# Optimization experiments

Hardware: AMD Instinct MI355X
Metric: run time of the kernel (lower is better)

## Reference

```python
import jax, jax.numpy as jnp
import numpy as np

# Fixed by module source / config defaults
L, H, D, DFF, T, B = 4, 4, 128, 512, 64, 1024
S, V, BOS = 4, 5, 4            # 4 orbital states, vocab 5, BOS token id 4
DH = D // H


def _ln(x, w, b):
    mu = x.mean(-1, keepdims=True)
    var = ((x - mu) ** 2).mean(-1, keepdims=True)
    return (x - mu) / jnp.sqrt(var + 1e-5) * w + b


def _decode(gumbel, state_emb, pos_emb, ln1_w, ln1_b, wqkv, bqkv, wo, bo,
            ln2_w, ln2_b, w1, b1, w2, b2, fn_w, fn_b, head_w, head_b,
            n_alpha, n_beta):
    def step(carry, xs):
        tok, a_rem, b_rem, Kc, Vc = carry
        g, i = xs                                   # g: (B,4), i: step index
        x = state_emb[tok] + pos_emb[i]             # (B, D)
        for l in range(L):
            # pre-LN causal self-attention with KV cache (torch MHA math)
            xn = _ln(x, ln1_w[l], ln1_b[l])
            q, k, v = jnp.split(xn @ wqkv[l].T + bqkv[l], 3, axis=-1)
            Kc = Kc.at[l, :, i].set(k)
            Vc = Vc.at[l, :, i].set(v)
            qh = q.reshape(B, H, DH)
            kh = Kc[l].reshape(B, T, H, DH)
            vh = Vc[l].reshape(B, T, H, DH)
            sc = jnp.einsum('bhd,bthd->bht', qh, kh) / jnp.sqrt(jnp.float32(DH))
            sc = jnp.where((jnp.arange(T) <= i)[None, None, :], sc, -jnp.inf)
            ctx = jnp.einsum('bht,bthd->bhd', jax.nn.softmax(sc, -1), vh).reshape(B, D)
            x = x + ctx @ wo[l].T + bo[l]
            # pre-LN FFN (exact GELU, matching nn.GELU default)
            h = jax.nn.gelu(_ln(x, ln2_w[l], ln2_b[l]) @ w1[l].T + b1[l], approximate=False)
            x = x + h @ w2[l].T + b2[l]
        logits = _ln(x, fn_w, fn_b) @ head_w.T + head_b   # (B, 4)
        # electron-budget validity mask (compute_validity_mask)
        oa = T - i - 1
        m = jnp.stack([
            (a_rem <= oa) & (b_rem <= oa),
            (b_rem > 0) & (a_rem <= oa) & (b_rem - 1 <= oa),
            (a_rem > 0) & (a_rem - 1 <= oa) & (b_rem <= oa),
            (a_rem > 0) & (b_rem > 0) & (a_rem - 1 <= oa) & (b_rem - 1 <= oa)], -1)
        logp = jax.nn.log_softmax(jnp.where(m, logits, -jnp.inf), -1)
        s = jnp.argmax(logp + g, -1)                # gumbel-max == multinomial
        lp = jnp.take_along_axis(logp, s[:, None], 1)[:, 0]
        return (s, a_rem - (s >> 1), b_rem - (s & 1), Kc, Vc), (s, lp)

    tok0 = jnp.full((B,), BOS, jnp.int32)
    a0 = jnp.full((B,), n_alpha, jnp.int32)
    b0 = jnp.full((B,), n_beta, jnp.int32)
    Kc0 = jnp.zeros((L, B, T, D), jnp.float32)
    Vc0 = jnp.zeros((L, B, T, D), jnp.float32)
    _, (states, lps) = jax.lax.scan(
        step, (tok0, a0, b0, Kc0, Vc0), (gumbel.transpose(1, 0, 2), jnp.arange(T)))
    return states.T, lps.sum(0)                      # (B, T) states, (B,) log-prob


def setup_inputs() -> dict:
    key = jax.random.key(0)
    ks = jax.random.split(key, 10)
    p = lambda k, shp: jax.random.normal(k, shp, jnp.float32) * 0.02
    u = jax.random.uniform(ks[0], (B, T, S), jnp.float32, 1e-6, 1.0 - 1e-6)
    return {
        'gumbel': -jnp.log(-jnp.log(u)),
        'state_emb': p(ks[1], (V, D)),
        'pos_emb': p(ks[2], (T + 1, D)),
        'ln1_w': jnp.ones((L, D)), 'ln1_b': jnp.zeros((L, D)),
        'wqkv': p(ks[3], (L, 3 * D, D)), 'bqkv': jnp.zeros((L, 3 * D)),
        'wo': p(ks[4], (L, D, D)), 'bo': jnp.zeros((L, D)),
        'ln2_w': jnp.ones((L, D)), 'ln2_b': jnp.zeros((L, D)),
        'w1': p(ks[5], (L, DFF, D)), 'b1': jnp.zeros((L, DFF)),
        'w2': p(ks[6], (L, D, DFF)), 'b2': jnp.zeros((L, D)),
        'fn_w': jnp.ones((D,)), 'fn_b': jnp.zeros((D,)),
        'head_w': p(ks[7], (S, D)), 'head_b': jnp.zeros((S,)),
        'n_alpha': 16, 'n_beta': 16,
    }


def reference(gumbel, state_emb, pos_emb, ln1_w, ln1_b, wqkv, bqkv, wo, bo,
              ln2_w, ln2_b, w1, b1, w2, b2, fn_w, fn_b, head_w, head_b,
              n_alpha, n_beta):
    return _decode(gumbel, state_emb, pos_emb, ln1_w, ln1_b, wqkv, bqkv, wo, bo,
                   ln2_w, ln2_b, w1, b1, w2, b2, fn_w, fn_b, head_w, head_b,
                   n_alpha, n_beta)
```

## Files before the change

### kernel.cpp

```cpp
#include <hip/hip_runtime.h>
#include <math.h>

namespace {
constexpr int L_ = 4, H_ = 4, D_ = 128, DFF_ = 512, T_ = 64, B_ = 1024;
constexpr int S_ = 4, BOS_ = 4, DH_ = 32;
constexpr int NB = 4;
constexpr int NBLK = B_ / NB;
constexpr int NTH = 1024;

constexpr size_t KC_BLK = (size_t)L_ * NB * T_ * D_;
constexpr size_t KC_OFF = 0;
constexpr size_t VC_OFF = KC_OFF + (size_t)NBLK * KC_BLK;
}

__device__ __forceinline__ float4 ld4(const float* p) {
  return *reinterpret_cast<const float4*>(p);
}

__device__ __forceinline__ float gelu_exact(float v) {
  return 0.5f * v * (1.0f + erff(v * 0.70710678118654752440f));
}

#define SEL4(a, e) ((e) == 0 ? (a)[0] : (e) == 1 ? (a)[1] : (e) == 2 ? (a)[2] : (a)[3])

__device__ __forceinline__ void ln_wave(const float* __restrict__ src,
                                        float* __restrict__ dst,
                                        const float* __restrict__ w,
                                        const float* __restrict__ b, int lane) {
  float v0 = src[lane], v1 = src[lane + 64];
  float s = v0 + v1;
#pragma unroll
  for (int off = 32; off > 0; off >>= 1) s += __shfl_xor(s, off);
  float mu = s * (1.f / 128.f);
  float d0 = v0 - mu, d1 = v1 - mu;
  float s2 = d0 * d0 + d1 * d1;
#pragma unroll
  for (int off = 32; off > 0; off >>= 1) s2 += __shfl_xor(s2, off);
  float inv = 1.f / sqrtf(s2 * (1.f / 128.f) + 1e-5f);
  dst[lane] = d0 * inv * w[lane] + b[lane];
  dst[lane + 64] = d1 * inv * w[lane + 64] + b[lane + 64];
}

__global__ __launch_bounds__(NTH) void decode_kernel(
    const float* __restrict__ gumbel, const float* __restrict__ state_emb,
    const float* __restrict__ pos_emb,
    const float* __restrict__ ln1w, const float* __restrict__ ln1b,
    const float* __restrict__ wqkv, const float* __restrict__ bqkv,
    const float* __restrict__ wo, const float* __restrict__ bo,
    const float* __restrict__ ln2w, const float* __restrict__ ln2b,
    const float* __restrict__ w1, const float* __restrict__ b1,
    const float* __restrict__ w2, const float* __restrict__ b2,
    const float* __restrict__ fnw, const float* __restrict__ fnb,
    const float* __restrict__ headw, const float* __restrict__ headb,
    const int* __restrict__ nalpha, const int* __restrict__ nbeta,
    float* __restrict__ ws, float* __restrict__ out) {
  const int tid = threadIdx.x;
  const int blk = blockIdx.x;
  const int lane = tid & 63;
  const int w = tid >> 6;
  const int og = tid >> 3;
  const int k8 = tid & 7;

  float* Kc = ws + KC_OFF + (size_t)blk * KC_BLK;
  float* Vc = ws + VC_OFF + (size_t)blk * KC_BLK;

  __shared__ __align__(16) float xres[NB][D_];
  __shared__ __align__(16) float xn[NB][D_];
  __shared__ __align__(16) float qb[NB][D_];
  __shared__ __align__(16) float hbuf[NB][DFF_];
  __shared__ float sc[NB][H_][T_];
  __shared__ float logits[NB][S_];
  __shared__ int tok[NB];

  int arem_r = 0, brem_r = 0;
  float lps_r = 0.f;
  if (tid < NB) {
    tok[tid] = BOS_;
    arem_r = nalpha[0];
    brem_r = nbeta[0];
  }
  __syncthreads();

  for (int i = 0; i < T_; ++i) {
    if (tid < 512) {
      const int e = tid >> 7, d = tid & 127;
      xres[e][d] = state_emb[tok[e] * D_ + d] + pos_emb[i * D_ + d];
    }
    __syncthreads();

    for (int l = 0; l < L_; ++l) {
      if (w < NB) ln_wave(xres[w], xn[w], ln1w + l * D_, ln1b + l * D_, lane);
      __syncthreads();

      {
        float aq[4] = {0.f, 0.f, 0.f, 0.f};
        float ak[4] = {0.f, 0.f, 0.f, 0.f};
        float av[4] = {0.f, 0.f, 0.f, 0.f};
        const float* wq = wqkv + ((size_t)l * 384 + og) * D_;
        const float* wk = wq + (size_t)128 * D_;
        const float* wv = wq + (size_t)256 * D_;
#pragma unroll
        for (int m = 0; m < 4; ++m) {
          const int f4 = k8 + 8 * m;
          const float4 q4 = ld4(wq + 4 * f4);
          const float4 k4v = ld4(wk + 4 * f4);
          const float4 v4 = ld4(wv + 4 * f4);
#pragma unroll
          for (int e = 0; e < 4; ++e) {
            const float4 x4 = ld4(&xn[e][4 * f4]);
            aq[e] += q4.x * x4.x + q4.y * x4.y + q4.z * x4.z + q4.w * x4.w;
            ak[e] += k4v.x * x4.x + k4v.y * x4.y + k4v.z * x4.z + k4v.w * x4.w;
            av[e] += v4.x * x4.x + v4.y * x4.y + v4.z * x4.z + v4.w * x4.w;
          }
        }
#pragma unroll
        for (int e = 0; e < 4; ++e) {
          aq[e] += __shfl_xor(aq[e], 1); aq[e] += __shfl_xor(aq[e], 2); aq[e] += __shfl_xor(aq[e], 4);
          ak[e] += __shfl_xor(ak[e], 1); ak[e] += __shfl_xor(ak[e], 2); ak[e] += __shfl_xor(ak[e], 4);
          av[e] += __shfl_xor(av[e], 1); av[e] += __shfl_xor(av[e], 2); av[e] += __shfl_xor(av[e], 4);
        }
        const size_t kvb = ((size_t)l * NB) * T_ * D_ + (size_t)i * D_ + og;
        if (k8 < 4) {
          const int e = k8;
          qb[e][og] = SEL4(aq, e) + bqkv[l * 384 + og];
          Vc[kvb + (size_t)e * T_ * D_] = SEL4(av, e) + bqkv[l * 384 + 256 + og];
        } else {
          const int e = k8 - 4;
          Kc[kvb + (size_t)e * T_ * D_] = SEL4(ak, e) + bqkv[l * 384 + 128 + og];
        }
      }
      __syncthreads();

      {
        const int e = w >> 2, h = w & 3;
        const int t = lane;
        float s0 = -INFINITY;
        {
          const float4* q4 = reinterpret_cast<const float4*>(&qb[e][h * DH_]);
          const float* kp = Kc + (((size_t)l * NB + e) * T_ + t) * D_ + h * DH_;
          float a = 0.f;
#pragma unroll
          for (int k = 0; k < 8; ++k) {
            const float4 qv = q4[k];
            const float4 kv = ld4(kp + 4 * k);
            a += qv.x * kv.x + qv.y * kv.y + qv.z * kv.z + qv.w * kv.w;
          }
          if (t <= i) s0 = a * 0.17677669529663687f;
        }
        float mx = s0;
#pragma unroll
        for (int off = 32; off > 0; off >>= 1) mx = fmaxf(mx, __shfl_xor(mx, off));
        float p = expf(s0 - mx);
        float sum = p;
#pragma unroll
        for (int off = 32; off > 0; off >>= 1) sum += __shfl_xor(sum, off);
        sc[e][h][t] = p / sum;

        const int j = lane & 31, thalf = lane >> 5;
        const float* vp = Vc + (((size_t)l * NB + e) * T_ + thalf * 32) * D_ + h * DH_ + j;
        const float* pp = &sc[e][h][thalf * 32];
        float acc = 0.f;
#pragma unroll
        for (int m2 = 0; m2 < 32; ++m2) {
          acc += pp[m2] * vp[(size_t)m2 * D_];
        }
        acc += __shfl_xor(acc, 32);
        if (thalf == 0) qb[e][h * DH_ + j] = acc;
      }
      __syncthreads();

      {
        float ac[4] = {0.f, 0.f, 0.f, 0.f};
        const float* wrow = wo + ((size_t)l * D_ + og) * D_;
#pragma unroll
        for (int m = 0; m < 4; ++m) {
          const int f4 = k8 + 8 * m;
          const float4 w4 = ld4(wrow + 4 * f4);
#pragma unroll
          for (int e = 0; e < 4; ++e) {
            const float4 x4 = ld4(&qb[e][4 * f4]);
            ac[e] += w4.x * x4.x + w4.y * x4.y + w4.z * x4.z + w4.w * x4.w;
          }
        }
#pragma unroll
        for (int e = 0; e < 4; ++e) {
          ac[e] += __shfl_xor(ac[e], 1); ac[e] += __shfl_xor(ac[e], 2); ac[e] += __shfl_xor(ac[e], 4);
        }
        if (k8 < 4) {
          const int e = k8;
          xres[e][og] += SEL4(ac, e) + bo[l * D_ + og];
        }
      }
      __syncthreads();

      if (w < NB) ln_wave(xres[w], xn[w], ln2w + l * D_, ln2b + l * D_, lane);
      __syncthreads();

      {
        float ac[4][4];
#pragma unroll
        for (int r = 0; r < 4; ++r)
#pragma unroll
          for (int e = 0; e < 4; ++e) ac[r][e] = 0.f;
        const float* wb = w1 + ((size_t)l * DFF_ + og) * D_;
#pragma unroll
        for (int m = 0; m < 4; ++m) {
          const int f4 = k8 + 8 * m;
          float4 wr[4];
#pragma unroll
          for (int r = 0; r < 4; ++r) wr[r] = ld4(wb + (size_t)(128 * r) * D_ + 4 * f4);
#pragma unroll
          for (int e = 0; e < 4; ++e) {
            const float4 x4 = ld4(&xn[e][4 * f4]);
#pragma unroll
            for (int r = 0; r < 4; ++r) {
              ac[r][e] += wr[r].x * x4.x + wr[r].y * x4.y + wr[r].z * x4.z + wr[r].w * x4.w;
            }
          }
        }
#pragma unroll
        for (int r = 0; r < 4; ++r)
#pragma unroll
          for (int e = 0; e < 4; ++e) {
            ac[r][e] += __shfl_xor(ac[r][e], 1);
            ac[r][e] += __shfl_xor(ac[r][e], 2);
            ac[r][e] += __shfl_xor(ac[r][e], 4);
          }
        if (k8 < 4) {
          const int e = k8;
          hbuf[e][og] = gelu_exact(SEL4(ac[0], e) + b1[l * DFF_ + og]);
          hbuf[e][og + 128] = gelu_exact(SEL4(ac[1], e) + b1[l * DFF_ + og + 128]);
        } else {
          const int e = k8 - 4;
          hbuf[e][og + 256] = gelu_exact(SEL4(ac[2], e) + b1[l * DFF_ + og + 256]);
          hbuf[e][og + 384] = gelu_exact(SEL4(ac[3], e) + b1[l * DFF_ + og + 384]);
        }
      }
      __syncthreads();

      {
        float ac[4] = {0.f, 0.f, 0.f, 0.f};
        const float* wrow = w2 + ((size_t)l * D_ + og) * DFF_;
#pragma unroll
        for (int m = 0; m < 16; ++m) {
          const int f4 = k8 + 8 * m;
          const float4 w4 = ld4(wrow + 4 * f4);
#pragma unroll
          for (int e = 0; e < 4; ++e) {
            const float4 h4 = ld4(&hbuf[e][4 * f4]);
            ac[e] += w4.x * h4.x + w4.y * h4.y + w4.z * h4.z + w4.w * h4.w;
          }
        }
#pragma unroll
        for (int e = 0; e < 4; ++e) {
          ac[e] += __shfl_xor(ac[e], 1); ac[e] += __shfl_xor(ac[e], 2); ac[e] += __shfl_xor(ac[e], 4);
        }
        if (k8 < 4) {
          const int e = k8;
          xres[e][og] += SEL4(ac, e) + b2[l * D_ + og];
        }
      }
      __syncthreads();
    }

    if (w < NB) ln_wave(xres[w], xn[w], fnw, fnb, lane);
    __syncthreads();

    if (tid < 512) {
      const int e = tid >> 7, rest = tid & 127, s = rest >> 5, j = rest & 31;
      const float4 a = ld4(&xn[e][4 * j]);
      const float4 hw = ld4(headw + s * D_ + 4 * j);
      float acc = a.x * hw.x + a.y * hw.y + a.z * hw.z + a.w * hw.w;
#pragma unroll
      for (int off = 1; off < 32; off <<= 1) acc += __shfl_xor(acc, off);
      if (j == 0) logits[e][s] = acc + headb[s];
    }
    __syncthreads();

    if (tid < NB) {
      const int e = tid;
      const int b = blk * NB + e;
      const int a = arem_r, bb = brem_r;
      const int oa = T_ - 1 - i;
      bool m[4];
      m[0] = (a <= oa) && (bb <= oa);
      m[1] = (bb > 0) && (a <= oa) && (bb - 1 <= oa);
      m[2] = (a > 0) && (a - 1 <= oa) && (bb <= oa);
      m[3] = (a > 0) && (bb > 0) && (a - 1 <= oa) && (bb - 1 <= oa);
      float mx = -INFINITY;
#pragma unroll
      for (int s = 0; s < 4; ++s)
        if (m[s]) mx = fmaxf(mx, logits[e][s]);
      float sum = 0.f;
      float lg[4];
#pragma unroll
      for (int s = 0; s < 4; ++s) {
        if (m[s]) {
          const float z = logits[e][s] - mx;
          sum += expf(z);
          lg[s] = z;
        } else {
          lg[s] = -INFINITY;
        }
      }
      const float lse = logf(sum);
      float best = -INFINITY;
      int bs = 0;
#pragma unroll
      for (int s = 0; s < 4; ++s) {
        const float lp = lg[s] - lse;
        const float y = lp + gumbel[((size_t)b * T_ + i) * S_ + s];
        if (y > best) { best = y; bs = s; }
      }
      lps_r += SEL4(lg, bs) - lse;
      out[(size_t)b * T_ + i] = (float)bs;
      tok[e] = bs;
      arem_r = a - (bs >> 1);
      brem_r = bb - (bs & 1);
    }
    __syncthreads();
  }

  if (tid < NB) out[(size_t)B_ * T_ + blk * NB + tid] = lps_r;
}

extern "C" void kernel_launch(void* const* d_in, const int* in_sizes, int n_in,
                              void* d_out, int out_size, void* d_ws, size_t ws_size,
                              hipStream_t stream) {
  const float* gumbel    = (const float*)d_in[0];
  const float* state_emb = (const float*)d_in[1];
  const float* pos_emb   = (const float*)d_in[2];
  const float* ln1w      = (const float*)d_in[3];
  const float* ln1b      = (const float*)d_in[4];
  const float* wqkv      = (const float*)d_in[5];
  const float* bqkv      = (const float*)d_in[6];
  const float* wo        = (const float*)d_in[7];
  const float* bo        = (const float*)d_in[8];
  const float* ln2w      = (const float*)d_in[9];
  const float* ln2b      = (const float*)d_in[10];
  const float* w1        = (const float*)d_in[11];
  const float* b1        = (const float*)d_in[12];
  const float* w2        = (const float*)d_in[13];
  const float* b2        = (const float*)d_in[14];
  const float* fnw       = (const float*)d_in[15];
  const float* fnb       = (const float*)d_in[16];
  const float* headw     = (const float*)d_in[17];
  const float* headb     = (const float*)d_in[18];
  const int* nalpha      = (const int*)d_in[19];
  const int* nbeta       = (const int*)d_in[20];
  float* ws = (float*)d_ws;
  float* out = (float*)d_out;

  decode_kernel<<<dim3(NBLK), dim3(NTH), 0, stream>>>(
      gumbel, state_emb, pos_emb, ln1w, ln1b, wqkv, bqkv, wo, bo, ln2w, ln2b,
      w1, b1, w2, b2, fnw, fnb, headw, headb, nalpha, nbeta, ws, out);
}
```

Baseline: 9.241 ms.

## Split block into per-sequence wave groups with atomic sub-barriers and head-major KV cache

Reassigns work so each group of four waves owns one sequence, with each wave handling one attention head and a slice of every projection. Block-wide __syncthreads are replaced by a spin barrier on a per-sequence shared-memory counter, so the four sequences in a block no longer wait on each other. The KV cache moves to a head-major layout so each wave's K/V rows are contiguous. Redundant layernorm and sampling now run in every wave, the attention loop skips masked timesteps, and the custom atomic barrier with sleep adds polling overhead and memory-ordering risk. Weight reuse also drops: each weight row is now loaded for one sequence instead of being shared across four.

```diff
diff --git a/kernel.cpp b/kernel.cpp
--- a/kernel.cpp
+++ b/kernel.cpp
@@ -8,9 +8,8 @@
 constexpr int NBLK = B_ / NB;
 constexpr int NTH = 1024;
 
-constexpr size_t KC_BLK = (size_t)L_ * NB * T_ * D_;
-constexpr size_t KC_OFF = 0;
-constexpr size_t VC_OFF = KC_OFF + (size_t)NBLK * KC_BLK;
+constexpr size_t KC_BLK = (size_t)L_ * NB * H_ * T_ * DH_;
+constexpr size_t VC_OFF = (size_t)NBLK * KC_BLK;
 }
 
 __device__ __forceinline__ float4 ld4(const float* p) {
@@ -23,10 +22,24 @@
 
 #define SEL4(a, e) ((e) == 0 ? (a)[0] : (e) == 1 ? (a)[1] : (e) == 2 ? (a)[2] : (a)[3])
 
-__device__ __forceinline__ void ln_wave(const float* __restrict__ src,
-                                        float* __restrict__ dst,
-                                        const float* __restrict__ w,
-                                        const float* __restrict__ b, int lane) {
+__device__ __forceinline__ void gbar(int* cnt, int lane) {
+  int tgt = 0;
+  if (lane == 0) {
+    int my = __hip_atomic_fetch_add(cnt, 1, __ATOMIC_RELEASE,
+                                    __HIP_MEMORY_SCOPE_WORKGROUP);
+    tgt = (my & ~3) + 4;
+  }
+  tgt = __shfl(tgt, 0);
+  while (__hip_atomic_load(cnt, __ATOMIC_ACQUIRE,
+                           __HIP_MEMORY_SCOPE_WORKGROUP) < tgt) {
+    __builtin_amdgcn_s_sleep(1);
+  }
+}
+
+__device__ __forceinline__ void ln_red(const float* __restrict__ src,
+                                       float* __restrict__ dst,
+                                       const float* __restrict__ w,
+                                       const float* __restrict__ b, int lane) {
   float v0 = src[lane], v1 = src[lane + 64];
   float s = v0 + v1;
 #pragma unroll
@@ -58,94 +71,105 @@
   const int blk = blockIdx.x;
   const int lane = tid & 63;
   const int w = tid >> 6;
-  const int og = tid >> 3;
-  const int k8 = tid & 7;
-
-  float* Kc = ws + KC_OFF + (size_t)blk * KC_BLK;
+  const int e = w >> 2;
+  const int h = w & 3;
+  const int og8 = lane >> 3;
+  const int k8 = lane & 7;
+
+  float* Kc = ws + (size_t)blk * KC_BLK;
   float* Vc = ws + VC_OFF + (size_t)blk * KC_BLK;
 
   __shared__ __align__(16) float xres[NB][D_];
   __shared__ __align__(16) float xn[NB][D_];
-  __shared__ __align__(16) float qb[NB][D_];
+  __shared__ __align__(16) float ctx[NB][D_];
   __shared__ __align__(16) float hbuf[NB][DFF_];
-  __shared__ float sc[NB][H_][T_];
+  __shared__ __align__(16) float qs[NB][H_][DH_];
+  __shared__ float ps[NB][H_][T_];
   __shared__ float logits[NB][S_];
-  __shared__ int tok[NB];
-
-  int arem_r = 0, brem_r = 0;
+  __shared__ int cnt[NB];
+
+  int bs_cur = BOS_;
+  int arem_r = nalpha[0], brem_r = nbeta[0];
   float lps_r = 0.f;
-  if (tid < NB) {
-    tok[tid] = BOS_;
-    arem_r = nalpha[0];
-    brem_r = nbeta[0];
-  }
+  if (tid < NB) cnt[tid] = 0;
   __syncthreads();
 
   for (int i = 0; i < T_; ++i) {
-    if (tid < 512) {
-      const int e = tid >> 7, d = tid & 127;
-      xres[e][d] = state_emb[tok[e] * D_ + d] + pos_emb[i * D_ + d];
+    if (lane < 32) {
+      const int d = h * 32 + lane;
+      xres[e][d] = state_emb[bs_cur * D_ + d] + pos_emb[i * D_ + d];
     }
-    __syncthreads();
+    gbar(&cnt[e], lane);
 
     for (int l = 0; l < L_; ++l) {
-      if (w < NB) ln_wave(xres[w], xn[w], ln1w + l * D_, ln1b + l * D_, lane);
-      __syncthreads();
+      ln_red(xres[e], xn[e], ln1w + l * D_, ln1b + l * D_, lane);
 
       {
-        float aq[4] = {0.f, 0.f, 0.f, 0.f};
-        float ak[4] = {0.f, 0.f, 0.f, 0.f};
-        float av[4] = {0.f, 0.f, 0.f, 0.f};
-        const float* wq = wqkv + ((size_t)l * 384 + og) * D_;
-        const float* wk = wq + (size_t)128 * D_;
-        const float* wv = wq + (size_t)256 * D_;
-#pragma unroll
-        for (int m = 0; m < 4; ++m) {
-          const int f4 = k8 + 8 * m;
-          const float4 q4 = ld4(wq + 4 * f4);
-          const float4 k4v = ld4(wk + 4 * f4);
-          const float4 v4 = ld4(wv + 4 * f4);
-#pragma unroll
-          for (int e = 0; e < 4; ++e) {
+        const float* wq = wqkv + ((size_t)l * 384 + h * 32) * D_;
+        const float* wk = wqkv + ((size_t)l * 384 + 128 + h * 32) * D_;
+        const float* wv = wqkv + ((size_t)l * 384 + 256 + h * 32) * D_;
+        const size_t cb = (((size_t)(l * NB + e) * H_ + h) * T_ + i) * DH_;
+#pragma unroll
+        for (int rg = 0; rg < 4; ++rg) {
+          const int r = rg * 8 + og8;
+          const float* wr = wq + (size_t)r * D_;
+          float acc = 0.f;
+#pragma unroll
+          for (int m = 0; m < 4; ++m) {
+            const int f4 = k8 + 8 * m;
+            const float4 w4 = ld4(wr + 4 * f4);
             const float4 x4 = ld4(&xn[e][4 * f4]);
-            aq[e] += q4.x * x4.x + q4.y * x4.y + q4.z * x4.z + q4.w * x4.w;
-            ak[e] += k4v.x * x4.x + k4v.y * x4.y + k4v.z * x4.z + k4v.w * x4.w;
-            av[e] += v4.x * x4.x + v4.y * x4.y + v4.z * x4.z + v4.w * x4.w;
+            acc += w4.x * x4.x + w4.y * x4.y + w4.z * x4.z + w4.w * x4.w;
           }
-        }
-#pragma unroll
-        for (int e = 0; e < 4; ++e) {
-          aq[e] += __shfl_xor(aq[e], 1); aq[e] += __shfl_xor(aq[e], 2); aq[e] += __shfl_xor(aq[e], 4);
-          ak[e] += __shfl_xor(ak[e], 1); ak[e] += __shfl_xor(ak[e], 2); ak[e] += __shfl_xor(ak[e], 4);
-          av[e] += __shfl_xor(av[e], 1); av[e] += __shfl_xor(av[e], 2); av[e] += __shfl_xor(av[e], 4);
-        }
-        const size_t kvb = ((size_t)l * NB) * T_ * D_ + (size_t)i * D_ + og;
-        if (k8 < 4) {
-          const int e = k8;
-          qb[e][og] = SEL4(aq, e) + bqkv[l * 384 + og];
-          Vc[kvb + (size_t)e * T_ * D_] = SEL4(av, e) + bqkv[l * 384 + 256 + og];
-        } else {
-          const int e = k8 - 4;
-          Kc[kvb + (size_t)e * T_ * D_] = SEL4(ak, e) + bqkv[l * 384 + 128 + og];
-        }
-      }
-      __syncthreads();
+          acc += __shfl_xor(acc, 1); acc += __shfl_xor(acc, 2); acc += __shfl_xor(acc, 4);
+          if (k8 == 0) qs[e][h][r] = acc + bqkv[l * 384 + h * 32 + r];
+        }
+#pragma unroll
+        for (int rg = 0; rg < 4; ++rg) {
+          const int r = rg * 8 + og8;
+          const float* wr = wk + (size_t)r * D_;
+          float acc = 0.f;
+#pragma unroll
+          for (int m = 0; m < 4; ++m) {
+            const int f4 = k8 + 8 * m;
+            const float4 w4 = ld4(wr + 4 * f4);
+            const float4 x4 = ld4(&xn[e][4 * f4]);
+            acc += w4.x * x4.x + w4.y * x4.y + w4.z * x4.z + w4.w * x4.w;
+          }
+          acc += __shfl_xor(acc, 1); acc += __shfl_xor(acc, 2); acc += __shfl_xor(acc, 4);
+          if (k8 == 0) Kc[cb + r] = acc + bqkv[l * 384 + 128 + h * 32 + r];
+        }
+#pragma unroll
+        for (int rg = 0; rg < 4; ++rg) {
+          const int r = rg * 8 + og8;
+          const float* wr = wv + (size_t)r * D_;
+          float acc = 0.f;
+#pragma unroll
+          for (int m = 0; m < 4; ++m) {
+            const int f4 = k8 + 8 * m;
+            const float4 w4 = ld4(wr + 4 * f4);
+            const float4 x4 = ld4(&xn[e][4 * f4]);
+            acc += w4.x * x4.x + w4.y * x4.y + w4.z * x4.z + w4.w * x4.w;
+          }
+          acc += __shfl_xor(acc, 1); acc += __shfl_xor(acc, 2); acc += __shfl_xor(acc, 4);
+          if (k8 == 0) Vc[cb + r] = acc + bqkv[l * 384 + 256 + h * 32 + r];
+        }
+      }
+      asm volatile("s_waitcnt vmcnt(0)" ::: "memory");
 
       {
-        const int e = w >> 2, h = w & 3;
         const int t = lane;
         float s0 = -INFINITY;
-        {
-          const float4* q4 = reinterpret_cast<const float4*>(&qb[e][h * DH_]);
-          const float* kp = Kc + (((size_t)l * NB + e) * T_ + t) * D_ + h * DH_;
+        if (t <= i) {
+          const float* kp = Kc + (((size_t)(l * NB + e) * H_ + h) * T_ + t) * DH_;
           float a = 0.f;
 #pragma unroll
           for (int k = 0; k < 8; ++k) {
-            const float4 qv = q4[k];
+            const float4 qv = ld4(&qs[e][h][4 * k]);
             const float4 kv = ld4(kp + 4 * k);
             a += qv.x * kv.x + qv.y * kv.y + qv.z * kv.z + qv.w * kv.w;
           }
-          if (t <= i) s0 = a * 0.17677669529663687f;
+          s0 = a * 0.17677669529663687f;
         }
         float mx = s0;
 #pragma unroll
@@ -154,148 +178,103 @@
         float sum = p;
 #pragma unroll
         for (int off = 32; off > 0; off >>= 1) sum += __shfl_xor(sum, off);
-        sc[e][h][t] = p / sum;
+        ps[e][h][t] = p / sum;
 
         const int j = lane & 31, thalf = lane >> 5;
-        const float* vp = Vc + (((size_t)l * NB + e) * T_ + thalf * 32) * D_ + h * DH_ + j;
-        const float* pp = &sc[e][h][thalf * 32];
+        const float* vp = Vc + (((size_t)(l * NB + e) * H_ + h) * T_) * DH_ + j;
+        const float* pp = &ps[e][h][thalf * 32];
         float acc = 0.f;
 #pragma unroll
-        for (int m2 = 0; m2 < 32; ++m2) {
-          acc += pp[m2] * vp[(size_t)m2 * D_];
+        for (int m = 0; m < 32; ++m) {
+          if (thalf * 32 + m <= i) acc += pp[m] * vp[(size_t)(thalf * 32 + m) * DH_];
         }
         acc += __shfl_xor(acc, 32);
-        if (thalf == 0) qb[e][h * DH_ + j] = acc;
-      }
-      __syncthreads();
-
-      {
-        float ac[4] = {0.f, 0.f, 0.f, 0.f};
-        const float* wrow = wo + ((size_t)l * D_ + og) * D_;
+        if (thalf == 0) ctx[e][h * 32 + j] = acc;
+      }
+      gbar(&cnt[e], lane);
+
+#pragma unroll
+      for (int rg = 0; rg < 4; ++rg) {
+        const int r = h * 32 + rg * 8 + og8;
+        const float* wr = wo + ((size_t)l * D_ + r) * D_;
+        float acc = 0.f;
 #pragma unroll
         for (int m = 0; m < 4; ++m) {
           const int f4 = k8 + 8 * m;
-          const float4 w4 = ld4(wrow + 4 * f4);
-#pragma unroll
-          for (int e = 0; e < 4; ++e) {
-            const float4 x4 = ld4(&qb[e][4 * f4]);
-            ac[e] += w4.x * x4.x + w4.y * x4.y + w4.z * x4.z + w4.w * x4.w;
-          }
-        }
-#pragma unroll
-        for (int e = 0; e < 4; ++e) {
-          ac[e] += __shfl_xor(ac[e], 1); ac[e] += __shfl_xor(ac[e], 2); ac[e] += __shfl_xor(ac[e], 4);
-        }
-        if (k8 < 4) {
-          const int e = k8;
-          xres[e][og] += SEL4(ac, e) + bo[l * D_ + og];
-        }
-      }
-      __syncthreads();
-
-      if (w < NB) ln_wave(xres[w], xn[w], ln2w + l * D_, ln2b + l * D_, lane);
-      __syncthreads();
-
-      {
-        float ac[4][4];
-#pragma unroll
-        for (int r = 0; r < 4; ++r)
-#pragma unroll
-          for (int e = 0; e < 4; ++e) ac[r][e] = 0.f;
-        const float* wb = w1 + ((size_t)l * DFF_ + og) * D_;
+          const float4 w4 = ld4(wr + 4 * f4);
+          const float4 x4 = ld4(&ctx[e][4 * f4]);
+          acc += w4.x * x4.x + w4.y * x4.y + w4.z * x4.z + w4.w * x4.w;
+        }
+        acc += __shfl_xor(acc, 1); acc += __shfl_xor(acc, 2); acc += __shfl_xor(acc, 4);
+        if (k8 == 0) xres[e][r] += acc + bo[l * D_ + r];
+      }
+      gbar(&cnt[e], lane);
+
+      ln_red(xres[e], xn[e], ln2w + l * D_, ln2b + l * D_, lane);
+
+#pragma unroll 4
+      for (int rg = 0; rg < 16; ++rg) {
+        const int r = h * 128 + rg * 8 + og8;
+        const float* wr = w1 + ((size_t)l * DFF_ + r) * D_;
+        float acc = 0.f;
 #pragma unroll
         for (int m = 0; m < 4; ++m) {
           const int f4 = k8 + 8 * m;
-          float4 wr[4];
-#pragma unroll
-          for (int r = 0; r < 4; ++r) wr[r] = ld4(wb + (size_t)(128 * r) * D_ + 4 * f4);
-#pragma unroll
-          for (int e = 0; e < 4; ++e) {
-            const float4 x4 = ld4(&xn[e][4 * f4]);
-#pragma unroll
-            for (int r = 0; r < 4; ++r) {
-              ac[r][e] += wr[r].x * x4.x + wr[r].y * x4.y + wr[r].z * x4.z + wr[r].w * x4.w;
-            }
-          }
-        }
-#pragma unroll
-        for (int r = 0; r < 4; ++r)
-#pragma unroll
-          for (int e = 0; e < 4; ++e) {
-            ac[r][e] += __shfl_xor(ac[r][e], 1);
-            ac[r][e] += __shfl_xor(ac[r][e], 2);
-            ac[r][e] += __shfl_xor(ac[r][e], 4);
-          }
-        if (k8 < 4) {
-          const int e = k8;
-          hbuf[e][og] = gelu_exact(SEL4(ac[0], e) + b1[l * DFF_ + og]);
-          hbuf[e][og + 128] = gelu_exact(SEL4(ac[1], e) + b1[l * DFF_ + og + 128]);
-        } else {
-          const int e = k8 - 4;
-          hbuf[e][og + 256] = gelu_exact(SEL4(ac[2], e) + b1[l * DFF_ + og + 256]);
-          hbuf[e][og + 384] = gelu_exact(SEL4(ac[3], e) + b1[l * DFF_ + og + 384]);
-        }
-      }
-      __syncthreads();
-
-      {
-        float ac[4] = {0.f, 0.f, 0.f, 0.f};
-        const float* wrow = w2 + ((size_t)l * D_ + og) * DFF_;
+          const float4 w4 = ld4(wr + 4 * f4);
+          const float4 x4 = ld4(&xn[e][4 * f4]);
+          acc += w4.x * x4.x + w4.y * x4.y + w4.z * x4.z + w4.w * x4.w;
+        }
+        acc += __shfl_xor(acc, 1); acc += __shfl_xor(acc, 2); acc += __shfl_xor(acc, 4);
+        if (k8 == 0) hbuf[e][r] = gelu_exact(acc + b1[l * DFF_ + r]);
+      }
+      gbar(&cnt[e], lane);
+
+#pragma unroll
+      for (int rg = 0; rg < 4; ++rg) {
+        const int r = h * 32 + rg * 8 + og8;
+        const float* wr = w2 + ((size_t)l * D_ + r) * DFF_;
+        float acc = 0.f;
 #pragma unroll
         for (int m = 0; m < 16; ++m) {
           const int f4 = k8 + 8 * m;
-          const float4 w4 = ld4(wrow + 4 * f4);
-#pragma unroll
-          for (int e = 0; e < 4; ++e) {
-            const float4 h4 = ld4(&hbuf[e][4 * f4]);
-            ac[e] += w4.x * h4.x + w4.y * h4.y + w4.z * h4.z + w4.w * h4.w;
-          }
-        }
-#pragma unroll
-        for (int e = 0; e < 4; ++e) {
-          ac[e] += __shfl_xor(ac[e], 1); ac[e] += __shfl_xor(ac[e], 2); ac[e] += __shfl_xor(ac[e], 4);
-        }
-        if (k8 < 4) {
-          const int e = k8;
-          xres[e][og] += SEL4(ac, e) + b2[l * D_ + og];
-        }
-      }
-      __syncthreads();
+          const float4 w4 = ld4(wr + 4 * f4);
+          const float4 x4 = ld4(&hbuf[e][4 * f4]);
+          acc += w4.x * x4.x + w4.y * x4.y + w4.z * x4.z + w4.w * x4.w;
+        }
+        acc += __shfl_xor(acc, 1); acc += __shfl_xor(acc, 2); acc += __shfl_xor(acc, 4);
+        if (k8 == 0) xres[e][r] += acc + b2[l * D_ + r];
+      }
+      gbar(&cnt[e], lane);
     }
 
-    if (w < NB) ln_wave(xres[w], xn[w], fnw, fnb, lane);
-    __syncthreads();
-
-    if (tid < 512) {
-      const int e = tid >> 7, rest = tid & 127, s = rest >> 5, j = rest & 31;
-      const float4 a = ld4(&xn[e][4 * j]);
-      const float4 hw = ld4(headw + s * D_ + 4 * j);
-      float acc = a.x * hw.x + a.y * hw.y + a.z * hw.z + a.w * hw.w;
-#pragma unroll
-      for (int off = 1; off < 32; off <<= 1) acc += __shfl_xor(acc, off);
-      if (j == 0) logits[e][s] = acc + headb[s];
+    ln_red(xres[e], xn[e], fnw, fnb, lane);
+
+    {
+      float v = xn[e][lane] * headw[h * D_ + lane] +
+                xn[e][lane + 64] * headw[h * D_ + lane + 64];
+#pragma unroll
+      for (int off = 32; off > 0; off >>= 1) v += __shfl_xor(v, off);
+      if (lane == 0) logits[e][h] = v + headb[h];
     }
-    __syncthreads();
-
-    if (tid < NB) {
-      const int e = tid;
-      const int b = blk * NB + e;
+    gbar(&cnt[e], lane);
+
+    {
       const int a = arem_r, bb = brem_r;
       const int oa = T_ - 1 - i;
-      bool m[4];
-      m[0] = (a <= oa) && (bb <= oa);
-      m[1] = (bb > 0) && (a <= oa) && (bb - 1 <= oa);
-      m[2] = (a > 0) && (a - 1 <= oa) && (bb <= oa);
-      m[3] = (a > 0) && (bb > 0) && (a - 1 <= oa) && (bb - 1 <= oa);
+      bool mk[4];
+      mk[0] = (a <= oa) && (bb <= oa);
+      mk[1] = (bb > 0) && (a <= oa) && (bb - 1 <= oa);
+      mk[2] = (a > 0) && (a - 1 <= oa) && (bb <= oa);
+      mk[3] = (a > 0) && (bb > 0) && (a - 1 <= oa) && (bb - 1 <= oa);
       float mx = -INFINITY;
 #pragma unroll
       for (int s = 0; s < 4; ++s)
-        if (m[s]) mx = fmaxf(mx, logits[e][s]);
+        if (mk[s]) mx = fmaxf(mx, logits[e][s]);
       float sum = 0.f;
       float lg[4];
 #pragma unroll
       for (int s = 0; s < 4; ++s) {
-        if (m[s]) {
+        if (mk[s]) {
           const float z = logits[e][s] - mx;
           sum += expf(z);
           lg[s] = z;
@@ -304,24 +283,23 @@
         }
       }
       const float lse = logf(sum);
+      const size_t gb = ((size_t)(blk * NB + e) * T_ + i) * S_;
       float best = -INFINITY;
       int bs = 0;
 #pragma unroll
       for (int s = 0; s < 4; ++s) {
-        const float lp = lg[s] - lse;
-        const float y = lp + gumbel[((size_t)b * T_ + i) * S_ + s];
+        const float y = (lg[s] - lse) + gumbel[gb + s];
         if (y > best) { best = y; bs = s; }
       }
       lps_r += SEL4(lg, bs) - lse;
-      out[(size_t)b * T_ + i] = (float)bs;
-      tok[e] = bs;
+      if (w == e * 4 && lane == 0) out[(size_t)(blk * NB + e) * T_ + i] = (float)bs;
+      bs_cur = bs;
       arem_r = a - (bs >> 1);
       brem_r = bb - (bs & 1);
     }
-    __syncthreads();
   }
 
-  if (tid < NB) out[(size_t)B_ * T_ + blk * NB + tid] = lps_r;
+  if (h == 0 && lane == 0) out[(size_t)B_ * T_ + blk * NB + e] = lps_r;
 }
 
 extern "C" void kernel_launch(void* const* d_in, const int* in_sizes, int n_in,
```

Result: slower. 22.88 ms (+147.6%).

## Halve sequences per block to two and skip masked causal attention work

Applied to the files above, without the earlier changes.

Each block now handles two sequences with 512 threads instead of four with 1024, giving 512 blocks. Every matvec is rewritten so each 8-lane group computes two output rows for both sequences. Attention also skips the QK dot products and the PV accumulation for positions past the current step. The aim is more blocks in flight and less wasted causal work, but weight rows are now re-read from cache for only two sequences per block instead of four.

```diff
diff --git a/kernel.cpp b/kernel.cpp
--- a/kernel.cpp
+++ b/kernel.cpp
@@ -4,13 +4,12 @@
 namespace {
 constexpr int L_ = 4, H_ = 4, D_ = 128, DFF_ = 512, T_ = 64, B_ = 1024;
 constexpr int S_ = 4, BOS_ = 4, DH_ = 32;
-constexpr int NB = 4;
+constexpr int NB = 2;
 constexpr int NBLK = B_ / NB;
-constexpr int NTH = 1024;
+constexpr int NTH = 512;
 
 constexpr size_t KC_BLK = (size_t)L_ * NB * T_ * D_;
-constexpr size_t KC_OFF = 0;
-constexpr size_t VC_OFF = KC_OFF + (size_t)NBLK * KC_BLK;
+constexpr size_t VC_OFF = (size_t)NBLK * KC_BLK;
 }
 
 __device__ __forceinline__ float4 ld4(const float* p) {
@@ -20,8 +19,6 @@
 __device__ __forceinline__ float gelu_exact(float v) {
   return 0.5f * v * (1.0f + erff(v * 0.70710678118654752440f));
 }
-
-#define SEL4(a, e) ((e) == 0 ? (a)[0] : (e) == 1 ? (a)[1] : (e) == 2 ? (a)[2] : (a)[3])
 
 __device__ __forceinline__ void ln_wave(const float* __restrict__ src,
                                         float* __restrict__ dst,
@@ -40,6 +37,8 @@
   dst[lane] = d0 * inv * w[lane] + b[lane];
   dst[lane + 64] = d1 * inv * w[lane + 64] + b[lane + 64];
 }
+
+#define RED8(a) { a += __shfl_xor(a, 1); a += __shfl_xor(a, 2); a += __shfl_xor(a, 4); }
 
 __global__ __launch_bounds__(NTH) void decode_kernel(
     const float* __restrict__ gumbel, const float* __restrict__ state_emb,
@@ -61,14 +60,14 @@
   const int og = tid >> 3;
   const int k8 = tid & 7;
 
-  float* Kc = ws + KC_OFF + (size_t)blk * KC_BLK;
+  float* Kc = ws + (size_t)blk * KC_BLK;
   float* Vc = ws + VC_OFF + (size_t)blk * KC_BLK;
 
   __shared__ __align__(16) float xres[NB][D_];
   __shared__ __align__(16) float xn[NB][D_];
   __shared__ __align__(16) float qb[NB][D_];
   __shared__ __align__(16) float hbuf[NB][DFF_];
-  __shared__ float sc[NB][H_][T_];
+  __shared__ float ps[NB][H_][T_];
   __shared__ float logits[NB][S_];
   __shared__ int tok[NB];
 
@@ -82,7 +81,7 @@
   __syncthreads();
 
   for (int i = 0; i < T_; ++i) {
-    if (tid < 512) {
+    if (tid < NB * D_) {
       const int e = tid >> 7, d = tid & 127;
       xres[e][d] = state_emb[tok[e] * D_ + d] + pos_emb[i * D_ + d];
     }
@@ -93,40 +92,54 @@
       __syncthreads();
 
       {
-        float aq[4] = {0.f, 0.f, 0.f, 0.f};
-        float ak[4] = {0.f, 0.f, 0.f, 0.f};
-        float av[4] = {0.f, 0.f, 0.f, 0.f};
-        const float* wq = wqkv + ((size_t)l * 384 + og) * D_;
-        const float* wk = wq + (size_t)128 * D_;
-        const float* wv = wq + (size_t)256 * D_;
+        float aq0[2] = {0.f, 0.f}, aq1[2] = {0.f, 0.f};
+        float ak0[2] = {0.f, 0.f}, ak1[2] = {0.f, 0.f};
+        float av0[2] = {0.f, 0.f}, av1[2] = {0.f, 0.f};
+        const float* wb = wqkv + (size_t)l * 384 * D_;
 #pragma unroll
         for (int m = 0; m < 4; ++m) {
           const int f4 = k8 + 8 * m;
-          const float4 q4 = ld4(wq + 4 * f4);
-          const float4 k4v = ld4(wk + 4 * f4);
-          const float4 v4 = ld4(wv + 4 * f4);
-#pragma unroll
-          for (int e = 0; e < 4; ++e) {
-            const float4 x4 = ld4(&xn[e][4 * f4]);
-            aq[e] += q4.x * x4.x + q4.y * x4.y + q4.z * x4.z + q4.w * x4.w;
-            ak[e] += k4v.x * x4.x + k4v.y * x4.y + k4v.z * x4.z + k4v.w * x4.w;
-            av[e] += v4.x * x4.x + v4.y * x4.y + v4.z * x4.z + v4.w * x4.w;
-          }
-        }
-#pragma unroll
-        for (int e = 0; e < 4; ++e) {
-          aq[e] += __shfl_xor(aq[e], 1); aq[e] += __shfl_xor(aq[e], 2); aq[e] += __shfl_xor(aq[e], 4);
-          ak[e] += __shfl_xor(ak[e], 1); ak[e] += __shfl_xor(ak[e], 2); ak[e] += __shfl_xor(ak[e], 4);
-          av[e] += __shfl_xor(av[e], 1); av[e] += __shfl_xor(av[e], 2); av[e] += __shfl_xor(av[e], 4);
-        }
-        const size_t kvb = ((size_t)l * NB) * T_ * D_ + (size_t)i * D_ + og;
-        if (k8 < 4) {
-          const int e = k8;
-          qb[e][og] = SEL4(aq, e) + bqkv[l * 384 + og];
-          Vc[kvb + (size_t)e * T_ * D_] = SEL4(av, e) + bqkv[l * 384 + 256 + og];
-        } else {
-          const int e = k8 - 4;
-          Kc[kvb + (size_t)e * T_ * D_] = SEL4(ak, e) + bqkv[l * 384 + 128 + og];
+          const float4 x0 = ld4(&xn[0][4 * f4]);
+          const float4 x1 = ld4(&xn[1][4 * f4]);
+          const float4 wq0 = ld4(wb + (size_t)(og) * D_ + 4 * f4);
+          const float4 wq1 = ld4(wb + (size_t)(og + 64) * D_ + 4 * f4);
+          const float4 wk0 = ld4(wb + (size_t)(og + 128) * D_ + 4 * f4);
+          const float4 wk1 = ld4(wb + (size_t)(og + 192) * D_ + 4 * f4);
+          const float4 wv0 = ld4(wb + (size_t)(og + 256) * D_ + 4 * f4);
+          const float4 wv1 = ld4(wb + (size_t)(og + 320) * D_ + 4 * f4);
+          aq0[0] += wq0.x * x0.x + wq0.y * x0.y + wq0.z * x0.z + wq0.w * x0.w;
+          aq0[1] += wq0.x * x1.x + wq0.y * x1.y + wq0.z * x1.z + wq0.w * x1.w;
+          aq1[0] += wq1.x * x0.x + wq1.y * x0.y + wq1.z * x0.z + wq1.w * x0.w;
+          aq1[1] += wq1.x * x1.x + wq1.y * x1.y + wq1.z * x1.z + wq1.w * x1.w;
+          ak0[0] += wk0.x * x0.x + wk0.y * x0.y + wk0.z * x0.z + wk0.w * x0.w;
+          ak0[1] += wk0.x * x1.x + wk0.y * x1.y + wk0.z * x1.z + wk0.w * x1.w;
+          ak1[0] += wk1.x * x0.x + wk1.y * x0.y + wk1.z * x0.z + wk1.w * x0.w;
+          ak1[1] += wk1.x * x1.x + wk1.y * x1.y + wk1.z * x1.z + wk1.w * x1.w;
+          av0[0] += wv0.x * x0.x + wv0.y * x0.y + wv0.z * x0.z + wv0.w * x0.w;
+          av0[1] += wv0.x * x1.x + wv0.y * x1.y + wv0.z * x1.z + wv0.w * x1.w;
+          av1[0] += wv1.x * x0.x + wv1.y * x0.y + wv1.z * x0.z + wv1.w * x0.w;
+          av1[1] += wv1.x * x1.x + wv1.y * x1.y + wv1.z * x1.z + wv1.w * x1.w;
+        }
+        RED8(aq0[0]); RED8(aq0[1]); RED8(aq1[0]); RED8(aq1[1]);
+        RED8(ak0[0]); RED8(ak0[1]); RED8(ak1[0]); RED8(ak1[1]);
+        RED8(av0[0]); RED8(av0[1]); RED8(av1[0]); RED8(av1[1]);
+        const float* bq = bqkv + l * 384;
+        if (k8 == 0) {
+          const size_t cb = (((size_t)l * NB + 0) * T_ + i) * D_;
+          qb[0][og] = aq0[0] + bq[og];
+          qb[0][og + 64] = aq1[0] + bq[og + 64];
+          Kc[cb + og] = ak0[0] + bq[og + 128];
+          Kc[cb + og + 64] = ak1[0] + bq[og + 192];
+          Vc[cb + og] = av0[0] + bq[og + 256];
+          Vc[cb + og + 64] = av1[0] + bq[og + 320];
+        } else if (k8 == 1) {
+          const size_t cb = (((size_t)l * NB + 1) * T_ + i) * D_;
+          qb[1][og] = aq0[1] + bq[og];
+          qb[1][og + 64] = aq1[1] + bq[og + 64];
+          Kc[cb + og] = ak0[1] + bq[og + 128];
+          Kc[cb + og + 64] = ak1[1] + bq[og + 192];
+          Vc[cb + og] = av0[1] + bq[og + 256];
+          Vc[cb + og + 64] = av1[1] + bq[og + 320];
         }
       }
       __syncthreads();
@@ -135,7 +148,7 @@
         const int e = w >> 2, h = w & 3;
         const int t = lane;
         float s0 = -INFINITY;
-        {
+        if (t <= i) {
           const float4* q4 = reinterpret_cast<const float4*>(&qb[e][h * DH_]);
           const float* kp = Kc + (((size_t)l * NB + e) * T_ + t) * D_ + h * DH_;
           float a = 0.f;
@@ -145,7 +158,7 @@
             const float4 kv = ld4(kp + 4 * k);
             a += qv.x * kv.x + qv.y * kv.y + qv.z * kv.z + qv.w * kv.w;
           }
-          if (t <= i) s0 = a * 0.17677669529663687f;
+          s0 = a * 0.17677669529663687f;
         }
         float mx = s0;
 #pragma unroll
@@ -154,15 +167,15 @@
         float sum = p;
 #pragma unroll
         for (int off = 32; off > 0; off >>= 1) sum += __shfl_xor(sum, off);
-        sc[e][h][t] = p / sum;
+        ps[e][h][t] = p / sum;
 
         const int j = lane & 31, thalf = lane >> 5;
         const float* vp = Vc + (((size_t)l * NB + e) * T_ + thalf * 32) * D_ + h * DH_ + j;
-        const float* pp = &sc[e][h][thalf * 32];
+        const float* pp = &ps[e][h][thalf * 32];
         float acc = 0.f;
 #pragma unroll
-        for (int m2 = 0; m2 < 32; ++m2) {
-          acc += pp[m2] * vp[(size_t)m2 * D_];
+        for (int m = 0; m < 32; ++m) {
+          if (thalf * 32 + m <= i) acc += pp[m] * vp[(size_t)m * D_];
         }
         acc += __shfl_xor(acc, 32);
         if (thalf == 0) qb[e][h * DH_ + j] = acc;
@@ -170,25 +183,27 @@
       __syncthreads();
 
       {
-        float ac[4] = {0.f, 0.f, 0.f, 0.f};
-        const float* wrow = wo + ((size_t)l * D_ + og) * D_;
+        float a0[2] = {0.f, 0.f}, a1[2] = {0.f, 0.f};
+        const float* wb = wo + (size_t)l * D_ * D_;
 #pragma unroll
         for (int m = 0; m < 4; ++m) {
           const int f4 = k8 + 8 * m;
-          const float4 w4 = ld4(wrow + 4 * f4);
-#pragma unroll
-          for (int e = 0; e < 4; ++e) {
-            const float4 x4 = ld4(&qb[e][4 * f4]);
-            ac[e] += w4.x * x4.x + w4.y * x4.y + w4.z * x4.z + w4.w * x4.w;
-          }
-        }
-#pragma unroll
-        for (int e = 0; e < 4; ++e) {
-          ac[e] += __shfl_xor(ac[e], 1); ac[e] += __shfl_xor(ac[e], 2); ac[e] += __shfl_xor(ac[e], 4);
-        }
-        if (k8 < 4) {
-          const int e = k8;
-          xres[e][og] += SEL4(ac, e) + bo[l * D_ + og];
+          const float4 x0 = ld4(&qb[0][4 * f4]);
+          const float4 x1 = ld4(&qb[1][4 * f4]);
+          const float4 w0 = ld4(wb + (size_t)(og) * D_ + 4 * f4);
+          const float4 w1v = ld4(wb + (size_t)(og + 64) * D_ + 4 * f4);
+          a0[0] += w0.x * x0.x + w0.y * x0.y + w0.z * x0.z + w0.w * x0.w;
+          a0[1] += w0.x * x1.x + w0.y * x1.y + w0.z * x1.z + w0.w * x1.w;
+          a1[0] += w1v.x * x0.x + w1v.y * x0.y + w1v.z * x0.z + w1v.w * x0.w;
+          a1[1] += w1v.x * x1.x + w1v.y * x1.y + w1v.z * x1.z + w1v.w * x1.w;
+        }
+        RED8(a0[0]); RED8(a0[1]); RED8(a1[0]); RED8(a1[1]);
+        if (k8 == 0) {
+          xres[0][og] += a0[0] + bo[l * D_ + og];
+          xres[0][og + 64] += a1[0] + bo[l * D_ + og + 64];
+        } else if (k8 == 1) {
+          xres[1][og] += a0[1] + bo[l * D_ + og];
+          xres[1][og + 64] += a1[1] + bo[l * D_ + og + 64];
         }
       }
       __syncthreads();
@@ -197,67 +212,62 @@
       __syncthreads();
 
       {
-        float ac[4][4];
-#pragma unroll
-        for (int r = 0; r < 4; ++r)
-#pragma unroll
-          for (int e = 0; e < 4; ++e) ac[r][e] = 0.f;
-        const float* wb = w1 + ((size_t)l * DFF_ + og) * D_;
+        float ac[8][2];
+#pragma unroll
+        for (int r = 0; r < 8; ++r) { ac[r][0] = 0.f; ac[r][1] = 0.f; }
+        const float* wb = w1 + (size_t)l * DFF_ * D_;
 #pragma unroll
         for (int m = 0; m < 4; ++m) {
           const int f4 = k8 + 8 * m;
-          float4 wr[4];
-#pragma unroll
-          for (int r = 0; r < 4; ++r) wr[r] = ld4(wb + (size_t)(128 * r) * D_ + 4 * f4);
-#pragma unroll
-          for (int e = 0; e < 4; ++e) {
-            const float4 x4 = ld4(&xn[e][4 * f4]);
-#pragma unroll
-            for (int r = 0; r < 4; ++r) {
-              ac[r][e] += wr[r].x * x4.x + wr[r].y * x4.y + wr[r].z * x4.z + wr[r].w * x4.w;
-            }
+          const float4 x0 = ld4(&xn[0][4 * f4]);
+          const float4 x1 = ld4(&xn[1][4 * f4]);
+#pragma unroll
+          for (int r = 0; r < 8; ++r) {
+            const float4 w4 = ld4(wb + (size_t)(og + 64 * r) * D_ + 4 * f4);
+            ac[r][0] += w4.x * x0.x + w4.y * x0.y + w4.z * x0.z + w4.w * x0.w;
+            ac[r][1] += w4.x * x1.x + w4.y * x1.y + w4.z * x1.z + w4.w * x1.w;
           }
         }
 #pragma unroll
-        for (int r = 0; r < 4; ++r)
-#pragma unroll
-          for (int e = 0; e < 4; ++e) {
-            ac[r][e] += __shfl_xor(ac[r][e], 1);
-            ac[r][e] += __shfl_xor(ac[r][e], 2);
-            ac[r][e] += __shfl_xor(ac[r][e], 4);
+        for (int r = 0; r < 8; ++r) { RED8(ac[r][0]); RED8(ac[r][1]); }
+        if (k8 == 0) {
+#pragma unroll
+          for (int r = 0; r < 8; ++r) {
+            const int o = og + 64 * r;
+            hbuf[0][o] = gelu_exact(ac[r][0] + b1[l * DFF_ + o]);
           }
-        if (k8 < 4) {
-          const int e = k8;
-          hbuf[e][og] = gelu_exact(SEL4(ac[0], e) + b1[l * DFF_ + og]);
-          hbuf[e][og + 128] = gelu_exact(SEL4(ac[1], e) + b1[l * DFF_ + og + 128]);
-        } else {
-          const int e = k8 - 4;
-          hbuf[e][og + 256] = gelu_exact(SEL4(ac[2], e) + b1[l * DFF_ + og + 256]);
-          hbuf[e][og + 384] = gelu_exact(SEL4(ac[3], e) + b1[l * DFF_ + og + 384]);
-        }
-      }
-      __syncthreads();
-
-      {
-        float ac[4] = {0.f, 0.f, 0.f, 0.f};
-        const float* wrow = w2 + ((size_t)l * D_ + og) * DFF_;
+        } else if (k8 == 1) {
+#pragma unroll
+          for (int r = 0; r < 8; ++r) {
+            const int o = og + 64 * r;
+            hbuf[1][o] = gelu_exact(ac[r][1] + b1[l * DFF_ + o]);
+          }
+        }
+      }
+      __syncthreads();
+
+      {
+        float a0[2] = {0.f, 0.f}, a1[2] = {0.f, 0.f};
+        const float* wb = w2 + (size_t)l * D_ * DFF_;
 #pragma unroll
         for (int m = 0; m < 16; ++m) {
           const int f4 = k8 + 8 * m;
-          const float4 w4 = ld4(wrow + 4 * f4);
-#pragma unroll
-          for (int e = 0; e < 4; ++e) {
-            const float4 h4 = ld4(&hbuf[e][4 * f4]);
-            ac[e] += w4.x * h4.x + w4.y * h4.y + w4.z * h4.z + w4.w * h4.w;
-          }
-        }
-#pragma unroll
-        for (int e = 0; e < 4; ++e) {
-          ac[e] += __shfl_xor(ac[e], 1); ac[e] += __shfl_xor(ac[e], 2); ac[e] += __shfl_xor(ac[e], 4);
-        }
-        if (k8 < 4) {
-          const int e = k8;
-          xres[e][og] += SEL4(ac, e) + b2[l * D_ + og];
+          const float4 h0 = ld4(&hbuf[0][4 * f4]);
+          const float4 h1 = ld4(&hbuf[1][4 * f4]);
+          const float4 w0 = ld4(wb + (size_t)(og) * DFF_ + 4 * f4);
+          const float4 w1v = ld4(wb + (size_t)(og + 64) * DFF_ + 4 * f4);
+          a0[0] += w0.x * h0.x + w0.y * h0.y + w0.z * h0.z + w0.w * h0.w;
+          a0[1] += w0.x * h1.x + w0.y * h1.y + w0.z * h1.z + w0.w * h1.w;
+          a1[0] += w1v.x * h0.x + w1v.y * h0.y + w1v.z * h0.z + w1v.w * h0.w;
+          a1[1] += w1v.x * h1.x + w1v.y * h1.y + w1v.z * h1.z + w1v.w * h1.w;
+        }
+        RED8(a0[0]); RED8(a0[1]); RED8(a1[0]); RED8(a1[1]);
+        if (k8 == 0) {
+          xres[0][og] += a0[0] + b2[l * D_ + og];
+          xres[0][og + 64] += a1[0] + b2[l * D_ + og + 64];
+        } else if (k8 == 1) {
+          xres[1][og] += a0[1] + b2[l * D_ + og];
+          xres[1][og + 64] += a1[1] + b2[l * D_ + og + 64];
         }
       }
       __syncthreads();
@@ -266,7 +276,7 @@
     if (w < NB) ln_wave(xres[w], xn[w], fnw, fnb, lane);
     __syncthreads();
 
-    if (tid < 512) {
+    if (tid < 256) {
       const int e = tid >> 7, rest = tid & 127, s = rest >> 5, j = rest & 31;
       const float4 a = ld4(&xn[e][4 * j]);
       const float4 hw = ld4(headw + s * D_ + 4 * j);
@@ -282,20 +292,20 @@
       const int b = blk * NB + e;
       const int a = arem_r, bb = brem_r;
       const int oa = T_ - 1 - i;
-      bool m[4];
-      m[0] = (a <= oa) && (bb <= oa);
-      m[1] = (bb > 0) && (a <= oa) && (bb - 1 <= oa);
-      m[2] = (a > 0) && (a - 1 <= oa) && (bb <= oa);
-      m[3] = (a > 0) && (bb > 0) && (a - 1 <= oa) && (bb - 1 <= oa);
+      bool mk[4];
+      mk[0] = (a <= oa) && (bb <= oa);
+      mk[1] = (bb > 0) && (a <= oa) && (bb - 1 <= oa);
+      mk[2] = (a > 0) && (a - 1 <= oa) && (bb <= oa);
+      mk[3] = (a > 0) && (bb > 0) && (a - 1 <= oa) && (bb - 1 <= oa);
       float mx = -INFINITY;
 #pragma unroll
       for (int s = 0; s < 4; ++s)
-        if (m[s]) mx = fmaxf(mx, logits[e][s]);
+        if (mk[s]) mx = fmaxf(mx, logits[e][s]);
       float sum = 0.f;
       float lg[4];
 #pragma unroll
       for (int s = 0; s < 4; ++s) {
-        if (m[s]) {
+        if (mk[s]) {
           const float z = logits[e][s] - mx;
           sum += expf(z);
           lg[s] = z;
@@ -308,11 +318,10 @@
       int bs = 0;
 #pragma unroll
       for (int s = 0; s < 4; ++s) {
-        const float lp = lg[s] - lse;
-        const float y = lp + gumbel[((size_t)b * T_ + i) * S_ + s];
+        const float y = (lg[s] - lse) + gumbel[((size_t)b * T_ + i) * S_ + s];
         if (y > best) { best = y; bs = s; }
       }
-      lps_r += SEL4(lg, bs) - lse;
+      lps_r += ((bs == 0) ? lg[0] : (bs == 1) ? lg[1] : (bs == 2) ? lg[2] : lg[3]) - lse;
       out[(size_t)b * T_ + i] = (float)bs;
       tok[e] = bs;
       arem_r = a - (bs >> 1);
```

Result: slower. 17.55 ms (+89.9%).
